# Performance work log

Hardware: AMD Instinct MI355X
Metric: run time of the kernel (lower is better)

## Reference

```python
import jax, jax.numpy as jnp
import numpy as np

T, H = 8192, 2048          # num_tokens, hidden_size
NH, NKV, D = 16, 4, 128    # num_heads, num_kv_heads, head_dim
R = 16                     # gate_low_rank_dim
NORM = 16.0                # gate_logit_normalizer
EPS = 1e-6                 # RMSNorm eps


def setup_inputs() -> dict:
    key = jax.random.key(0)
    ks = jax.random.split(key, 8)
    rnd = lambda k, sh, f: jax.random.normal(k, sh, dtype=jnp.float32) * f
    return {
        "hidden_states": rnd(ks[0], (T, H), 1.0),
        "Wqkv": rnd(ks[1], (H, (NH + 2 * NKV) * D), 0.02),
        "bqkv": rnd(ks[2], ((NH + 2 * NKV) * D,), 0.02),
        "gk_w0": rnd(ks[3], (H, R), 0.02),
        "gk_w1": rnd(ks[4], (R, NKV * D), 0.02),
        "gk_b1": rnd(ks[5], (NKV * D,), 0.02),
        "gnorm_w": jnp.ones((D,), jnp.float32),
        "Wo": rnd(ks[6], (NH * D, H), 0.02),
    }


def _gla_scan(q, k, v, g):
    # q,k,v,g: [NH, T, D]. State S: [D, D] per head.
    def step(S, x):
        qt, kt, vt, gt = x
        S = jnp.exp(gt)[:, None] * S + kt[:, None] * vt[None, :]
        return S, qt @ S

    def per_head(qh, kh, vh, gh):
        S0 = jnp.zeros((D, D), qh.dtype)
        _, o = jax.lax.scan(step, S0, (qh, kh, vh, gh))
        return o  # [T, D]

    return jax.vmap(per_head)(q, k, v, g)  # [NH, T, D]


def reference(hidden_states, Wqkv, bqkv, gk_w0, gk_w1, gk_b1, gnorm_w, Wo):
    # qkv projection (with bias), split into q / k / v
    qkv = hidden_states @ Wqkv + bqkv                    # [T, (NH+2*NKV)*D]
    q, k, v = jnp.split(qkv, [NH * D, NH * D + NKV * D], axis=-1)
    # low-rank gate projection (bias0=False, bias1=True)
    gk = (hidden_states @ gk_w0) @ gk_w1 + gk_b1         # [T, NKV*D]

    q = jax.nn.relu(q).reshape(T, NH, D)                 # feature_map = relu
    k = jax.nn.relu(k).reshape(T, NKV, D)
    v = v.reshape(T, NKV, D)
    gk = jax.nn.log_sigmoid(gk).reshape(T, NKV, D) / NORM

    # GQA: repeat_interleave kv heads to NH heads
    rep = NH // NKV
    k = jnp.repeat(k, rep, axis=1)
    v = jnp.repeat(v, rep, axis=1)
    gk = jnp.repeat(gk, rep, axis=1)

    q = q * (D ** -0.5)                                  # fused_chunk_gla default scale

    qh, kh, vh, gh = (t.transpose(1, 0, 2) for t in (q, k, v, gk))  # [NH, T, D]
    o = _gla_scan(qh, kh, vh, gh)                        # [NH, T, D]

    # per-head RMSNorm over head_dim
    o = o * jax.lax.rsqrt(jnp.mean(o * o, axis=-1, keepdims=True) + EPS) * gnorm_w

    o = o.transpose(1, 0, 2).reshape(T, NH * D)          # h n d -> n (h d)
    return o @ Wo                                        # o_proj (no bias)
```

## Files before the change

kernel.cpp:

```cpp
#include <hip/hip_runtime.h>
#include <hip/hip_bf16.h>
#include <cstdint>

typedef unsigned short u16;
typedef unsigned int u32;
typedef float f32x4 __attribute__((ext_vector_type(4)));
typedef short bf16x8 __attribute__((ext_vector_type(8)));

#define T_TOK 8192
#define HID 2048
#define NH 16
#define NKV 4
#define HD 128
#define QKVN 3072
#define CHUNK 64
#define NC 128

__device__ __forceinline__ float bf2f(u16 h){
  u32 u = ((u32)h) << 16;
  return __builtin_bit_cast(float, u);
}
__device__ __forceinline__ u16 f2bf(float f){
  u32 u = __builtin_bit_cast(u32, f);
  u32 r = (u + 0x7fffu + ((u >> 16) & 1u)) >> 16;
  return (u16)r;
}
__device__ __forceinline__ u32 pack2(float a, float b){
  return (u32)f2bf(a) | ((u32)f2bf(b) << 16);
}
__device__ __forceinline__ void gl2lds16(const u16* g, u16* l){
  __builtin_amdgcn_global_load_lds(
      (const __attribute__((address_space(1))) u32*)g,
      (__attribute__((address_space(3))) u32*)l, 16, 0, 0);
}

__global__ __launch_bounds__(256) void cvt_f2b_kernel(
    const float* __restrict__ in, u16* __restrict__ out, int n8)
{
  int i = blockIdx.x*256 + threadIdx.x;
  if (i >= n8) return;
  const float4* p = (const float4*)(in + (size_t)i*8);
  float4 a = p[0], b = p[1];
  uint4 pk;
  pk.x = pack2(a.x, a.y); pk.y = pack2(a.z, a.w);
  pk.z = pack2(b.x, b.y); pk.w = pack2(b.z, b.w);
  *(uint4*)(out + (size_t)i*8) = pk;
}

#define BM 256
#define BN 128
#define BK 64
#define NBUF 3
#define ABUF (BM*BK)
#define BBUF (BN*BK)
#define BUFU (ABUF + BBUF)

__device__ __forceinline__ int swz(int o){ return o ^ (((o >> 7) & 7) << 4); }

__device__ __forceinline__ void stage16(const u16* g, int ldg, u16* l, int o){
  int p = o ^ (((o >> 7) & 7) << 4);
  gl2lds16(g + (size_t)(p >> 7) * ldg + ((p >> 1) & 63), l + (o >> 1));
}

template<typename YT>
__global__ __launch_bounds__(512, 2) void gemm_8ph(
    const u16* __restrict__ X, const u16* __restrict__ Wt,
    const float* __restrict__ bias, const float* __restrict__ ebuf,
    const float* __restrict__ rbuf, YT* __restrict__ Y,
    int M, int N, int K, int mode)
{
  __shared__ u16 lds[NBUF * BUFU];
  const int tid  = threadIdx.x;
  const int lane = tid & 63;
  const int wave = tid >> 6;
  const int wm = wave >> 1;
  const int wn = wave & 1;
  const int ml = lane & 15, q8 = (lane >> 4) << 3;

  const int MT = M >> 8;
  const int nwg = gridDim.x;
  const int q = nwg >> 3, r = nwg & 7;
  const int xcd = blockIdx.x & 7, loc = blockIdx.x >> 3;
  const int wg = ((xcd < r) ? xcd * (q + 1) : r * (q + 1) + (xcd - r) * q) + loc;
  const int bm0 = (wg % MT) * BM;
  const int bn0 = (wg / MT) * BN;

  const u16* gA = X  + (size_t)bm0 * K;
  const u16* gB = Wt + (size_t)bn0 * K;

  f32x4 acc[4][4];
  #pragma unroll
  for (int i = 0; i < 4; i++)
    #pragma unroll
    for (int j = 0; j < 4; j++) acc[i][j] = f32x4{0.f, 0.f, 0.f, 0.f};

  const int NT = K >> 6;

  #pragma unroll
  for (int t = 0; t < 2; ++t){
    u16* La = lds + t * BUFU;
    u16* Lb = La + ABUF;
    const u16* ga = gA + t * BK;
    const u16* gb = gB + t * BK;
    #pragma unroll
    for (int it = 0; it < 4; ++it) stage16(ga, K, La, (it * 512 + tid) * 16);
    #pragma unroll
    for (int it = 0; it < 2; ++it) stage16(gb, K, Lb, (it * 512 + tid) * 16);
  }
  asm volatile("s_waitcnt vmcnt(6)" ::: "memory");
  __syncthreads();

  for (int t = 0; t < NT; ++t){
    u16* La = lds + (t % NBUF) * BUFU;
    u16* Lb = La + ABUF;
    const int ts = t + 2;
    const bool do_stage = ts < NT;
    u16* Sa = lds + (ts % NBUF) * BUFU;
    u16* Sb = Sa + ABUF;
    const u16* ga = gA + ts * BK;
    const u16* gb = gB + ts * BK;

    #pragma unroll
    for (int kk = 0; kk < 2; ++kk){
      bf16x8 af[4], bfr[4];
      #pragma unroll
      for (int i = 0; i < 4; ++i){
        int rowA = wm * 64 + i * 16 + ml;
        af[i] = *(const bf16x8*)((const char*)La + swz(rowA * 128 + (kk * 32 + q8) * 2));
      }
      #pragma unroll
      for (int j = 0; j < 4; ++j){
        int rowB = wn * 64 + j * 16 + ml;
        bfr[j] = *(const bf16x8*)((const char*)Lb + swz(rowB * 128 + (kk * 32 + q8) * 2));
      }
      if (do_stage){
        stage16(ga, K, Sa, ((kk * 2 + 0) * 512 + tid) * 16);
        stage16(ga, K, Sa, ((kk * 2 + 1) * 512 + tid) * 16);
        stage16(gb, K, Sb, (kk * 512 + tid) * 16);
      }
      __builtin_amdgcn_sched_barrier(0);
      __builtin_amdgcn_s_barrier();
      asm volatile("s_waitcnt lgkmcnt(0)" ::: "memory");
      __builtin_amdgcn_sched_barrier(0);
      __builtin_amdgcn_s_setprio(1);
      #pragma unroll
      for (int i = 0; i < 4; ++i)
        #pragma unroll
        for (int j = 0; j < 4; ++j)
          acc[i][j] = __builtin_amdgcn_mfma_f32_16x16x32_bf16(af[i], bfr[j], acc[i][j], 0, 0, 0);
      __builtin_amdgcn_s_setprio(0);
      if (kk == 1){
        if (ts < NT)         asm volatile("s_waitcnt vmcnt(6)" ::: "memory");
        else if (t + 1 < NT) asm volatile("s_waitcnt vmcnt(0)" ::: "memory");
      }
      __builtin_amdgcn_s_barrier();
    }
  }

  #pragma unroll
  for (int i = 0; i < 4; i++){
    int row = bm0 + wm * 64 + i * 16 + (lane >> 4) * 4;
    #pragma unroll
    for (int j = 0; j < 4; j++){
      int col = bn0 + wn * 64 + j * 16 + (lane & 15);
      float bv = 0.f;
      if (mode == 1) bv = bias[col];
      #pragma unroll
      for (int rr2 = 0; rr2 < 4; rr2++){
        float v = acc[i][j][rr2] + bv;
        if (mode == 1){
          int token = row + rr2;
          int cc = token >> 6, tt = token & 63, ii = col & 127;
          if (col < 2048){
            v = fmaxf(v, 0.f) * 0.08838834764831845f;
            v *= ebuf[(((size_t)cc*4 + (col>>9))*64 + tt)*128 + ii];
          } else if (col < 2560){
            v = fmaxf(v, 0.f);
            v *= rbuf[(((size_t)cc*4 + ((col-2048)>>7))*64 + tt)*128 + ii];
          }
        }
        if (sizeof(YT) == 2) Y[(size_t)(row+rr2)*N + col] = (YT)f2bf(v);
        else                 Y[(size_t)(row+rr2)*N + col] = (YT)v;
      }
    }
  }
}

__global__ __launch_bounds__(256) void transpose_f2b(
    const float* __restrict__ in, u16* __restrict__ out, int R, int C)
{
  __shared__ float tile[32][33];
  int c0 = blockIdx.x*32, r0 = blockIdx.y*32;
  int tx = threadIdx.x & 31, ty = threadIdx.x >> 5;
  #pragma unroll
  for (int p=0;p<4;p++) tile[ty + p*8][tx] = in[(size_t)(r0 + ty + p*8)*C + c0 + tx];
  __syncthreads();
  #pragma unroll
  for (int p=0;p<4;p++) out[(size_t)(c0 + ty + p*8)*R + r0 + tx] = f2bf(tile[tx][ty + p*8]);
}

__global__ __launch_bounds__(256) void gk1_kernel(
    const u16* __restrict__ hsb, const float* __restrict__ w0, float* __restrict__ tmp)
{
  int row = blockIdx.x*4 + (threadIdx.x >> 6);
  int lane = threadIdx.x & 63;
  float acc[16];
  #pragma unroll
  for (int n=0;n<16;n++) acc[n]=0.f;
  for (int k = lane; k < HID; k += 64){
    float h = bf2f(hsb[(size_t)row*HID + k]);
    const float* wr = w0 + (size_t)k*16;
    #pragma unroll
    for (int q=0;q<4;q++){
      float4 wv = *(const float4*)(wr + q*4);
      acc[q*4+0] += h*wv.x; acc[q*4+1] += h*wv.y;
      acc[q*4+2] += h*wv.z; acc[q*4+3] += h*wv.w;
    }
  }
  #pragma unroll
  for (int n=0;n<16;n++){
    #pragma unroll
    for (int off=32; off>0; off>>=1)
      acc[n] += __shfl_down(acc[n], off);
  }
  if (lane == 0){
    #pragma unroll
    for (int n=0;n<16;n++) tmp[(size_t)row*16 + n] = acc[n];
  }
}

__global__ __launch_bounds__(256) void gk2_kernel(
    const float* __restrict__ tmp, const float* __restrict__ w1,
    const float* __restrict__ b1, float* __restrict__ g)
{
  int id = blockIdx.x*256 + threadIdx.x;
  int rrow = id >> 9, n = id & 511;
  float a = b1[n];
  #pragma unroll
  for (int k=0;k<16;k++)
    a += tmp[(size_t)rrow*16 + k] * w1[k*512 + n];
  float ls = fminf(a, 0.f) - log1pf(__expf(-fabsf(a)));
  g[id] = ls * 0.0625f;
}

__global__ __launch_bounds__(256) void decay_kernel(
    const float* __restrict__ g, float* __restrict__ ebuf,
    float* __restrict__ rbuf, float* __restrict__ expB)
{
  __shared__ float bL[CHUNK*HD];
  const int c = blockIdx.x, h = blockIdx.y, tid = threadIdx.x;
  for (int off = tid; off < CHUNK*HD; off += 256){
    int t = off >> 7, i = off & 127;
    bL[off] = g[(size_t)(c*CHUNK + t)*512 + h*HD + i];
  }
  __syncthreads();
  if (tid < HD){
    float run = 0.f;
    for (int t=0;t<CHUNK;t++){ run += bL[t*HD + tid]; bL[t*HD + tid] = run; }
    expB[(size_t)(c*NKV + h)*HD + tid] = __expf(run);
  }
  __syncthreads();
  size_t base = (size_t)(c*NKV + h)*CHUNK*HD;
  for (int off = tid; off < CHUNK*HD; off += 256){
    float b = bL[off];
    ebuf[base + off] = __expf(b);
    rbuf[base + off] = __expf(-b);
  }
}

__global__ __launch_bounds__(256) void chunk_stats2_kernel(
    const u16* __restrict__ qkv, const float* __restrict__ expB,
    u16* __restrict__ Kt, u16* __restrict__ Vt)
{
  __shared__ u16 kL[CHUNK*HD];
  __shared__ u16 vL[CHUNK*HD];
  const int c = blockIdx.x, h = blockIdx.y, tid = threadIdx.x;
  #pragma unroll
  for (int it=0; it<4; it++){
    int u = it*256 + tid;
    int t = u >> 4, p = (u & 15)*8;
    size_t tok = (size_t)(c*CHUNK + t);
    *(uint4*)(kL + t*HD + p) = *(const uint4*)(qkv + tok*QKVN + 2048 + h*HD + p);
    *(uint4*)(vL + t*HD + p) = *(const uint4*)(qkv + tok*QKVN + 2560 + h*HD + p);
  }
  __syncthreads();
  {
    int j = tid >> 1, sh = (tid & 1)*32;
    u16* dst = Vt + ((size_t)(c*NKV + h)*HD + j)*CHUNK + sh;
    #pragma unroll
    for (int s2=0; s2<16; s2++){
      u32 a = (u32)vL[(sh + 2*s2)*HD + j] | ((u32)vL[(sh + 2*s2 + 1)*HD + j] << 16);
      *(u32*)(dst + 2*s2) = a;
    }
  }
  int jj = tid >> 1, ih = (tid & 1)*64;
  float acc[64];
  #pragma unroll
  for (int z=0;z<64;z++) acc[z]=0.f;
  for (int t=0;t<CHUNK;t++){
    float vj = bf2f(vL[t*HD + jj]);
    const u32* kp = (const u32*)(kL + t*HD + ih);
    #pragma unroll
    for (int z2=0; z2<32; z2++){
      u32 kw = kp[z2];
      acc[2*z2]   += vj * bf2f((u16)(kw & 0xffffu));
      acc[2*z2+1] += vj * bf2f((u16)(kw >> 16));
    }
  }
  u16* kout = Kt + ((size_t)(c*NKV + h)*HD + jj)*HD + ih;
  const float* eB = expB + (size_t)(c*NKV + h)*HD + ih;
  #pragma unroll
  for (int z2=0; z2<32; z2++)
    *(u32*)(kout + 2*z2) = pack2(acc[2*z2]*eB[2*z2], acc[2*z2+1]*eB[2*z2+1]);
}

__global__ __launch_bounds__(256) void state_scan2_kernel(
    const u16* __restrict__ Kt, const float* __restrict__ expB, u16* __restrict__ St)
{
  int wid = blockIdx.x;
  int h = wid >> 6;
  int j = (wid & 63)*2 + (threadIdx.x >> 7);
  int i = threadIdx.x & 127;
  size_t base = ((size_t)h*HD + j)*HD + i;
  float S = 0.f;
  for (int cc=0; cc<NC; cc++){
    size_t off = (size_t)cc*(NKV*HD*HD) + base;
    St[off] = f2bf(S);
    S = expB[((size_t)cc*NKV + h)*HD + i] * S + bf2f(Kt[off]);
  }
}

__global__ __launch_bounds__(256) void attn_fused_kernel(
    const u16* __restrict__ qkv, const u16* __restrict__ St,
    const u16* __restrict__ Vt, const float* __restrict__ gw,
    u16* __restrict__ obuf)
{
  __shared__ u16 qe[64*136];
  __shared__ u16 kb[64*136];
  __shared__ u16 sb[64*136];
  __shared__ u16 vb[128*72];
  __shared__ u16 pb[64*72];
  const int c = blockIdx.x, qh = blockIdx.y, h = qh >> 2;
  const int tid = threadIdx.x, lane = tid & 63, w = tid >> 6;
  const int ml = lane & 15, quad = lane >> 4, q8 = quad * 8;

  #pragma unroll
  for (int it = 0; it < 4; it++){
    int u = it*256 + tid;
    int t = u >> 4, p = (u & 15) * 8;
    size_t tok = (size_t)(c*CHUNK + t);
    *(uint4*)(qe + t*136 + p) = *(const uint4*)(qkv + tok*QKVN + qh*HD + p);
    *(uint4*)(kb + t*136 + p) = *(const uint4*)(qkv + tok*QKVN + 2048 + h*HD + p);
  }
  __syncthreads();

  bf16x8 aq[4];
  #pragma unroll
  for (int kk=0;kk<4;kk++)
    aq[kk] = *(const bf16x8*)(qe + (w*16 + ml)*136 + kk*32 + q8);
  #pragma unroll
  for (int n=0;n<4;n++){
    f32x4 pa = {0.f,0.f,0.f,0.f};
    #pragma unroll
    for (int kk=0;kk<4;kk++){
      bf16x8 bk = *(const bf16x8*)(kb + (n*16 + ml)*136 + kk*32 + q8);
      pa = __builtin_amdgcn_mfma_f32_16x16x32_bf16(aq[kk], bk, pa, 0, 0, 0);
    }
    #pragma unroll
    for (int r=0;r<4;r++){
      int ti = quad*4 + r;
      float v = (w*16 + ti >= n*16 + ml) ? pa[r] : 0.f;
      pb[(w*16 + ti)*72 + n*16 + ml] = f2bf(v);
    }
  }
  #pragma unroll
  for (int it = 0; it < 4; it++){
    int u = it*256 + tid;
    int j = u >> 3, p = (u & 7) * 8;
    *(uint4*)(vb + j*72 + p) =
        *(const uint4*)(Vt + ((size_t)(c*NKV + h)*HD + j)*CHUNK + p);
    int t2 = u >> 4, p2 = (u & 15) * 8;
    *(uint4*)(sb + t2*136 + p2) =
        *(const uint4*)(St + ((size_t)(c*NKV + h)*HD + t2)*HD + p2);
  }
  __syncthreads();

  f32x4 o[8];
  #pragma unroll
  for (int n=0;n<8;n++) o[n] = f32x4{0.f,0.f,0.f,0.f};
  bf16x8 ap[2];
  #pragma unroll
  for (int ks=0;ks<2;ks++)
    ap[ks] = *(const bf16x8*)(pb + (w*16 + ml)*72 + ks*32 + q8);
  #pragma unroll
  for (int n=0;n<8;n++)
    #pragma unroll
    for (int ks=0;ks<2;ks++){
      bf16x8 bv = *(const bf16x8*)(vb + (n*16 + ml)*72 + ks*32 + q8);
      o[n] = __builtin_amdgcn_mfma_f32_16x16x32_bf16(ap[ks], bv, o[n], 0, 0, 0);
    }
  #pragma unroll
  for (int n=0;n<4;n++)
    #pragma unroll
    for (int kk=0;kk<4;kk++){
      bf16x8 bs = *(const bf16x8*)(sb + (n*16 + ml)*136 + kk*32 + q8);
      o[n] = __builtin_amdgcn_mfma_f32_16x16x32_bf16(aq[kk], bs, o[n], 0, 0, 0);
    }
  #pragma unroll
  for (int it = 0; it < 4; it++){
    int u = it*256 + tid;
    int t2 = u >> 4, p2 = (u & 15) * 8;
    *(uint4*)(kb + t2*136 + p2) =
        *(const uint4*)(St + ((size_t)(c*NKV + h)*HD + 64 + t2)*HD + p2);
  }
  __syncthreads();
  #pragma unroll
  for (int n=0;n<4;n++)
    #pragma unroll
    for (int kk=0;kk<4;kk++){
      bf16x8 bs = *(const bf16x8*)(kb + (n*16 + ml)*136 + kk*32 + q8);
      o[4+n] = __builtin_amdgcn_mfma_f32_16x16x32_bf16(aq[kk], bs, o[4+n], 0, 0, 0);
    }

  float rstd[4];
  #pragma unroll
  for (int r=0;r<4;r++){
    float s = 0.f;
    #pragma unroll
    for (int n=0;n<8;n++) s += o[n][r]*o[n][r];
    #pragma unroll
    for (int off=1; off<16; off<<=1) s += __shfl_xor(s, off);
    rstd[r] = rsqrtf(s*(1.f/128.f) + 1e-6f);
  }
  #pragma unroll
  for (int n=0;n<8;n++){
    float gwv = gw[n*16 + ml];
    #pragma unroll
    for (int r=0;r<4;r++){
      int t = w*16 + quad*4 + r;
      float val = o[n][r] * rstd[r] * gwv;
      obuf[(size_t)(c*CHUNK + t)*(NH*HD) + qh*HD + n*16 + ml] = f2bf(val);
    }
  }
}

extern "C" void kernel_launch(void* const* d_in, const int* in_sizes, int n_in,
                              void* d_out, int out_size, void* d_ws, size_t ws_size,
                              hipStream_t stream)
{
  const float* hs   = (const float*)d_in[0];
  const float* Wqkv = (const float*)d_in[1];
  const float* bqkv = (const float*)d_in[2];
  const float* w0   = (const float*)d_in[3];
  const float* w1   = (const float*)d_in[4];
  const float* b1   = (const float*)d_in[5];
  const float* gw   = (const float*)d_in[6];
  const float* Wo   = (const float*)d_in[7];
  float* out = (float*)d_out;

  char* ws = (char*)d_ws;
  size_t off = 0;
  auto alloc = [&](size_t bytes)->char*{
    char* p = ws + off; off += (bytes + 255) & ~(size_t)255; return p;
  };
  u16*   hsb   = (u16*)  alloc((size_t)T_TOK*HID*2);
  u16*   Wt1   = (u16*)  alloc((size_t)QKVN*HID*2);
  u16*   Wt2   = (u16*)  alloc((size_t)HID*HID*2);
  u16*   qkv   = (u16*)  alloc((size_t)T_TOK*QKVN*2);
  float* gtmp  = (float*)alloc((size_t)T_TOK*16*4);
  float* g     = (float*)alloc((size_t)T_TOK*512*4);
  float* ebuf  = (float*)alloc((size_t)NC*NKV*CHUNK*HD*4);
  float* rbuf  = (float*)alloc((size_t)NC*NKV*CHUNK*HD*4);
  float* expB  = (float*)alloc((size_t)NC*NKV*HD*4);
  u16*   Kt    = (u16*)  alloc((size_t)NC*NKV*HD*HD*2);
  u16*   St    = (u16*)  alloc((size_t)NC*NKV*HD*HD*2);
  u16*   Vt    = (u16*)  alloc((size_t)NC*NKV*HD*CHUNK*2);
  u16*   obuf  = (u16*)  alloc((size_t)T_TOK*NH*HD*2);

  cvt_f2b_kernel<<<dim3(T_TOK*HID/8/256), 256, 0, stream>>>(hs, hsb, T_TOK*HID/8);
  transpose_f2b<<<dim3(QKVN/32, HID/32), 256, 0, stream>>>(Wqkv, Wt1, HID, QKVN);
  transpose_f2b<<<dim3(HID/32,  HID/32), 256, 0, stream>>>(Wo,   Wt2, HID, HID);
  gk1_kernel<<<dim3(T_TOK/4), 256, 0, stream>>>(hsb, w0, gtmp);
  gk2_kernel<<<dim3(T_TOK*512/256), 256, 0, stream>>>(gtmp, w1, b1, g);
  decay_kernel<<<dim3(NC, NKV), 256, 0, stream>>>(g, ebuf, rbuf, expB);
  gemm_8ph<u16><<<dim3((T_TOK/BM)*(QKVN/BN)), 512, 0, stream>>>(
      hsb, Wt1, bqkv, ebuf, rbuf, qkv, T_TOK, QKVN, HID, 1);
  chunk_stats2_kernel<<<dim3(NC, NKV), 256, 0, stream>>>(qkv, expB, Kt, Vt);
  state_scan2_kernel<<<dim3(256), 256, 0, stream>>>(Kt, expB, St);
  attn_fused_kernel<<<dim3(NC, NH), 256, 0, stream>>>(qkv, St, Vt, gw, obuf);
  gemm_8ph<float><<<dim3((T_TOK/BM)*(HID/BN)), 512, 0, stream>>>(
      obuf, Wt2, nullptr, nullptr, nullptr, out, T_TOK, HID, HID, 0);
}
```

Measured before the change: 599.6 us.

## Enlarge GEMM tiles to 256x256 with double-buffered half-tile staging

The bf16 MFMA GEMM kernel moves from a 256x128 tile with triple buffering to a 256x256 tile with double buffering. Waves are rearranged 2x4, and each wave computes two 64-row halves, so each B fragment loaded from LDS is reused across 8 MFMA row blocks. Global-to-LDS staging is split into half-tiles interleaved with the compute phases, and the workgroup-to-XCD mapping becomes row-major chunking. The aim is higher arithmetic intensity and fewer global loads per FLOP. The costs are a larger accumulator register file, which can hurt occupancy at 2 blocks per CU given 64KB LDS per buffer pair, and fewer workgroups in the grid.

```diff
diff --git a/kernel.cpp b/kernel.cpp
--- a/kernel.cpp
+++ b/kernel.cpp
@@ -48,9 +48,8 @@
 }
 
 #define BM 256
-#define BN 128
+#define BN 256
 #define BK 64
-#define NBUF 3
 #define ABUF (BM*BK)
 #define BBUF (BN*BK)
 #define BUFU (ABUF + BBUF)
@@ -62,81 +61,79 @@
   gl2lds16(g + (size_t)(p >> 7) * ldg + ((p >> 1) & 63), l + (o >> 1));
 }
 
+__device__ __forceinline__ void stage_half(const u16* g, int ldg, u16* lregion,
+                                           int half, int tid){
+  stage16(g, ldg, lregion, (half*1024 + tid)*16);
+  stage16(g, ldg, lregion, (half*1024 + 512 + tid)*16);
+}
+
 template<typename YT>
-__global__ __launch_bounds__(512, 2) void gemm_8ph(
+__global__ __launch_bounds__(512, 2) void gemm_v2(
     const u16* __restrict__ X, const u16* __restrict__ Wt,
     const float* __restrict__ bias, const float* __restrict__ ebuf,
     const float* __restrict__ rbuf, YT* __restrict__ Y,
     int M, int N, int K, int mode)
 {
-  __shared__ u16 lds[NBUF * BUFU];
+  __shared__ u16 lds[2 * BUFU];
   const int tid  = threadIdx.x;
   const int lane = tid & 63;
   const int wave = tid >> 6;
-  const int wm = wave >> 1;
-  const int wn = wave & 1;
-  const int ml = lane & 15, q8 = (lane >> 4) << 3;
-
-  const int MT = M >> 8;
+  const int wm = wave >> 2;
+  const int wn = wave & 3;
+  const int ml = lane & 15, quad = lane >> 4;
+
   const int nwg = gridDim.x;
-  const int q = nwg >> 3, r = nwg & 7;
-  const int xcd = blockIdx.x & 7, loc = blockIdx.x >> 3;
-  const int wg = ((xcd < r) ? xcd * (q + 1) : r * (q + 1) + (xcd - r) * q) + loc;
-  const int bm0 = (wg % MT) * BM;
-  const int bn0 = (wg / MT) * BN;
+  const int chunk = nwg >> 3;
+  const int lg = (blockIdx.x & 7) * chunk + (blockIdx.x >> 3);
+  const int NBt = N >> 8;
+  const int bm0 = (lg / NBt) * BM;
+  const int bn0 = (lg % NBt) * BN;
 
   const u16* gA = X  + (size_t)bm0 * K;
   const u16* gB = Wt + (size_t)bn0 * K;
 
-  f32x4 acc[4][4];
-  #pragma unroll
-  for (int i = 0; i < 4; i++)
+  f32x4 acc[8][4];
+  #pragma unroll
+  for (int i = 0; i < 8; i++)
     #pragma unroll
     for (int j = 0; j < 4; j++) acc[i][j] = f32x4{0.f, 0.f, 0.f, 0.f};
 
   const int NT = K >> 6;
 
-  #pragma unroll
-  for (int t = 0; t < 2; ++t){
-    u16* La = lds + t * BUFU;
+  auto ldfrag = [&](const u16* base, int row, int kk)->bf16x8{
+    return *(const bf16x8*)((const char*)base + swz(row*128 + kk*64 + quad*16));
+  };
+
+  {
+    u16* La0 = lds;
+    u16* Lb0 = lds + ABUF;
+    stage_half(gB, K, Lb0, 0, tid);
+    stage_half(gB, K, Lb0, 1, tid);
+    stage_half(gA, K, La0, 0, tid);
+    stage_half(gA, K, La0, 1, tid);
+  }
+  asm volatile("s_waitcnt vmcnt(2)" ::: "memory");
+  __builtin_amdgcn_s_barrier();
+
+  for (int t = 0; t < NT; ++t){
+    u16* La = lds + (t & 1) * BUFU;
     u16* Lb = La + ABUF;
-    const u16* ga = gA + t * BK;
-    const u16* gb = gB + t * BK;
-    #pragma unroll
-    for (int it = 0; it < 4; ++it) stage16(ga, K, La, (it * 512 + tid) * 16);
-    #pragma unroll
-    for (int it = 0; it < 2; ++it) stage16(gb, K, Lb, (it * 512 + tid) * 16);
-  }
-  asm volatile("s_waitcnt vmcnt(6)" ::: "memory");
-  __syncthreads();
-
-  for (int t = 0; t < NT; ++t){
-    u16* La = lds + (t % NBUF) * BUFU;
-    u16* Lb = La + ABUF;
-    const int ts = t + 2;
-    const bool do_stage = ts < NT;
-    u16* Sa = lds + (ts % NBUF) * BUFU;
-    u16* Sb = Sa + ABUF;
-    const u16* ga = gA + ts * BK;
-    const u16* gb = gB + ts * BK;
+    u16* Na = lds + ((t + 1) & 1) * BUFU;
+    u16* Nb = Na + ABUF;
+    const u16* ga = gA + (t + 1) * BK;
+    const u16* gb = gB + (t + 1) * BK;
+    const bool st = (t + 1 < NT);
 
     #pragma unroll
     for (int kk = 0; kk < 2; ++kk){
       bf16x8 af[4], bfr[4];
       #pragma unroll
-      for (int i = 0; i < 4; ++i){
-        int rowA = wm * 64 + i * 16 + ml;
-        af[i] = *(const bf16x8*)((const char*)La + swz(rowA * 128 + (kk * 32 + q8) * 2));
-      }
+      for (int j = 0; j < 4; ++j) bfr[j] = ldfrag(Lb, wn*64 + j*16 + ml, kk);
       #pragma unroll
-      for (int j = 0; j < 4; ++j){
-        int rowB = wn * 64 + j * 16 + ml;
-        bfr[j] = *(const bf16x8*)((const char*)Lb + swz(rowB * 128 + (kk * 32 + q8) * 2));
-      }
-      if (do_stage){
-        stage16(ga, K, Sa, ((kk * 2 + 0) * 512 + tid) * 16);
-        stage16(ga, K, Sa, ((kk * 2 + 1) * 512 + tid) * 16);
-        stage16(gb, K, Sb, (kk * 512 + tid) * 16);
+      for (int i = 0; i < 4; ++i) af[i] = ldfrag(La, wm*64 + i*16 + ml, kk);
+      if (st){
+        if (kk == 0) stage_half(gb, K, Nb, 0, tid);
+        else         stage_half(ga, K, Na, 0, tid);
       }
       __builtin_amdgcn_sched_barrier(0);
       __builtin_amdgcn_s_barrier();
@@ -149,38 +146,62 @@
         for (int j = 0; j < 4; ++j)
           acc[i][j] = __builtin_amdgcn_mfma_f32_16x16x32_bf16(af[i], bfr[j], acc[i][j], 0, 0, 0);
       __builtin_amdgcn_s_setprio(0);
-      if (kk == 1){
-        if (ts < NT)         asm volatile("s_waitcnt vmcnt(6)" ::: "memory");
-        else if (t + 1 < NT) asm volatile("s_waitcnt vmcnt(0)" ::: "memory");
+      if (kk == 0){
+        if (st) asm volatile("s_waitcnt vmcnt(2)" ::: "memory");
+        else    asm volatile("s_waitcnt vmcnt(0)" ::: "memory");
       }
       __builtin_amdgcn_s_barrier();
-    }
-  }
-
-  #pragma unroll
-  for (int i = 0; i < 4; i++){
-    int row = bm0 + wm * 64 + i * 16 + (lane >> 4) * 4;
-    #pragma unroll
-    for (int j = 0; j < 4; j++){
-      int col = bn0 + wn * 64 + j * 16 + (lane & 15);
-      float bv = 0.f;
-      if (mode == 1) bv = bias[col];
+
       #pragma unroll
-      for (int rr2 = 0; rr2 < 4; rr2++){
-        float v = acc[i][j][rr2] + bv;
-        if (mode == 1){
-          int token = row + rr2;
-          int cc = token >> 6, tt = token & 63, ii = col & 127;
-          if (col < 2048){
-            v = fmaxf(v, 0.f) * 0.08838834764831845f;
-            v *= ebuf[(((size_t)cc*4 + (col>>9))*64 + tt)*128 + ii];
-          } else if (col < 2560){
-            v = fmaxf(v, 0.f);
-            v *= rbuf[(((size_t)cc*4 + ((col-2048)>>7))*64 + tt)*128 + ii];
+      for (int i = 0; i < 4; ++i) af[i] = ldfrag(La, 128 + wm*64 + i*16 + ml, kk);
+      if (st){
+        if (kk == 0) stage_half(gb, K, Nb, 1, tid);
+        else         stage_half(ga, K, Na, 1, tid);
+      }
+      __builtin_amdgcn_sched_barrier(0);
+      __builtin_amdgcn_s_barrier();
+      asm volatile("s_waitcnt lgkmcnt(0)" ::: "memory");
+      __builtin_amdgcn_sched_barrier(0);
+      __builtin_amdgcn_s_setprio(1);
+      #pragma unroll
+      for (int i = 0; i < 4; ++i)
+        #pragma unroll
+        for (int j = 0; j < 4; ++j)
+          acc[4+i][j] = __builtin_amdgcn_mfma_f32_16x16x32_bf16(af[i], bfr[j], acc[4+i][j], 0, 0, 0);
+      __builtin_amdgcn_s_setprio(0);
+      if (kk == 1 && st)
+        asm volatile("s_waitcnt vmcnt(2)" ::: "memory");
+      __builtin_amdgcn_s_barrier();
+    }
+  }
+
+  #pragma unroll
+  for (int rh = 0; rh < 2; rh++){
+    #pragma unroll
+    for (int i = 0; i < 4; i++){
+      int row = bm0 + rh*128 + wm*64 + i*16 + quad*4;
+      #pragma unroll
+      for (int j = 0; j < 4; j++){
+        int col = bn0 + wn*64 + j*16 + ml;
+        float bv = 0.f;
+        if (mode == 1) bv = bias[col];
+        #pragma unroll
+        for (int rr2 = 0; rr2 < 4; rr2++){
+          float v = acc[rh*4+i][j][rr2] + bv;
+          if (mode == 1){
+            int token = row + rr2;
+            int cc = token >> 6, tt = token & 63, ii = col & 127;
+            if (col < 2048){
+              v = fmaxf(v, 0.f) * 0.08838834764831845f;
+              v *= ebuf[(((size_t)cc*4 + (col>>9))*64 + tt)*128 + ii];
+            } else if (col < 2560){
+              v = fmaxf(v, 0.f);
+              v *= rbuf[(((size_t)cc*4 + ((col-2048)>>7))*64 + tt)*128 + ii];
+            }
           }
+          if (sizeof(YT) == 2) Y[(size_t)(row+rr2)*N + col] = (YT)f2bf(v);
+          else                 Y[(size_t)(row+rr2)*N + col] = (YT)v;
         }
-        if (sizeof(YT) == 2) Y[(size_t)(row+rr2)*N + col] = (YT)f2bf(v);
-        else                 Y[(size_t)(row+rr2)*N + col] = (YT)v;
       }
     }
   }
@@ -483,11 +504,11 @@
   gk1_kernel<<<dim3(T_TOK/4), 256, 0, stream>>>(hsb, w0, gtmp);
   gk2_kernel<<<dim3(T_TOK*512/256), 256, 0, stream>>>(gtmp, w1, b1, g);
   decay_kernel<<<dim3(NC, NKV), 256, 0, stream>>>(g, ebuf, rbuf, expB);
-  gemm_8ph<u16><<<dim3((T_TOK/BM)*(QKVN/BN)), 512, 0, stream>>>(
+  gemm_v2<u16><<<dim3((T_TOK/BM)*(QKVN/BN)), 512, 0, stream>>>(
       hsb, Wt1, bqkv, ebuf, rbuf, qkv, T_TOK, QKVN, HID, 1);
   chunk_stats2_kernel<<<dim3(NC, NKV), 256, 0, stream>>>(qkv, expB, Kt, Vt);
   state_scan2_kernel<<<dim3(256), 256, 0, stream>>>(Kt, expB, St);
   attn_fused_kernel<<<dim3(NC, NH), 256, 0, stream>>>(qkv, St, Vt, gw, obuf);
-  gemm_8ph<float><<<dim3((T_TOK/BM)*(HID/BN)), 512, 0, stream>>>(
+  gemm_v2<float><<<dim3((T_TOK/BM)*(HID/BN)), 512, 0, stream>>>(
       obuf, Wt2, nullptr, nullptr, nullptr, out, T_TOK, HID, HID, 0);
 }
```

After: 600.4 us. No clear change (+0.1%).
